# Performance work log

Hardware: AMD Instinct MI355X
Metric: run time of the kernel (lower is better)

## Reference

```python
import jax, jax.numpy as jnp
import numpy as np

EPS = 1e-5

def layer_norm(h, g, b):
    m = h.mean(-1, keepdims=True)
    v = ((h - m) ** 2).mean(-1, keepdims=True)
    return (h - m) * jax.lax.rsqrt(v + EPS) * g + b

def setup_inputs() -> dict:
    key = jax.random.key(0)
    ks = jax.random.split(key, 16)
    B, D, C, H, EH, L = 64, 20000, 16, 64, 128, 32
    s = lambda k, fan_in, shape: jax.random.normal(k, shape, jnp.float32) / np.sqrt(fan_in)
    return {
        "x": jax.random.normal(ks[0], (B, D), jnp.float32),
        "mask": jax.random.randint(ks[1], (B, D), 0, 2, jnp.int32),
        "feature_embedding": jax.random.normal(ks[2], (D, C), jnp.float32),
        # h_layer: Linear(1+C -> H), LN, ReLU, Linear(H -> C), LN, ReLU
        "W1": s(ks[3], 1 + C, (1 + C, H)), "b1": jnp.zeros((H,), jnp.float32),
        "g1": jnp.ones((H,), jnp.float32), "be1": jnp.zeros((H,), jnp.float32),
        "W2": s(ks[4], H, (H, C)), "b2": jnp.zeros((C,), jnp.float32),
        "g2": jnp.ones((C,), jnp.float32), "be2": jnp.zeros((C,), jnp.float32),
        # encoder_mlp (FCLayers, 2 layers, LayerNorm + ReLU each): C -> EH -> 2L
        "We1": s(ks[5], C, (C, EH)), "bb1": jnp.zeros((EH,), jnp.float32),
        "gg1": jnp.ones((EH,), jnp.float32), "bbe1": jnp.zeros((EH,), jnp.float32),
        "We2": s(ks[6], EH, (EH, 2 * L)), "bb2": jnp.zeros((2 * L,), jnp.float32),
        "gg2": jnp.ones((2 * L,), jnp.float32), "bbe2": jnp.zeros((2 * L,), jnp.float32),
    }

def reference(x, mask, feature_embedding, W1, b1, g1, be1, W2, b2, g2, be2,
              We1, bb1, gg1, bbe1, We2, bb2, gg2, bbe2):
    B, D = x.shape
    C = feature_embedding.shape[1]
    # per-feature point-net: h_layer runs row-wise, so we compute it densely
    # for all (b, d) and zero out unobserved entries before pooling —
    # identical math to the per-sample masked gather in the original.
    h_in = jnp.concatenate(
        [x[..., None], jnp.broadcast_to(feature_embedding, (B, D, C))], axis=-1
    )  # [B, D, 1+C]
    h = jax.nn.relu(layer_norm(h_in @ W1 + b1, g1, be1))   # [B, D, H]
    h = jax.nn.relu(layer_norm(h @ W2 + b2, g2, be2))      # [B, D, C]
    m = mask.astype(h.dtype)
    summed = jnp.einsum('bdc,bd->bc', h, m)                # masked sum pool
    num_obs = jnp.maximum(m.sum(axis=1, keepdims=True), 1.0)
    c = summed / num_obs                                   # pool_mode='mean'
    # encoder_mlp
    e = jax.nn.relu(layer_norm(c @ We1 + bb1, gg1, bbe1))
    e = jax.nn.relu(layer_norm(e @ We2 + bb2, gg2, bbe2))  # [B, 2*latent]
    mu, logvar = jnp.split(e, 2, axis=-1)
    return mu, logvar
```

## Files before the change

kernel.cpp:

```cpp
#include <hip/hip_runtime.h>
#include <hip/hip_bf16.h>

#define EPSF 1e-5f

namespace {
constexpr int B = 64, D = 20000, C = 16, H = 64, EH = 128, L = 32;
constexpr int CHUNK = 256;
constexpr int NCHUNK = (D + CHUNK - 1) / CHUNK;
constexpr int GX = 12;
}

typedef __attribute__((ext_vector_type(8))) short bf16x8;
typedef __attribute__((ext_vector_type(4))) float f32x4;

static __device__ __forceinline__ unsigned short f2bf(float f) {
    __hip_bfloat16 h = __float2bfloat16(f);
    return __builtin_bit_cast(unsigned short, h);
}
static __device__ __forceinline__ unsigned int packbf(float lo, float hi) {
    return ((unsigned int)f2bf(hi) << 16) | (unsigned int)f2bf(lo);
}

__global__ __launch_bounds__(256) void k_count_prep(
    const int* __restrict__ mask, const float* __restrict__ fe,
    const float* __restrict__ W1, const float* __restrict__ b1,
    const float* __restrict__ W2,
    int* __restrict__ chunkpop, unsigned short* __restrict__ febf,
    unsigned short* __restrict__ W1T, unsigned short* __restrict__ W2T)
{
    const int j = blockIdx.x, b = blockIdx.y;
    const int t = threadIdx.x;
    if (j < NCHUNK) {
        const int d = j * CHUNK + t;
        const int mv = (d < D) ? mask[(size_t)b * D + d] : 0;
        const unsigned long long bal = __ballot(mv != 0);
        __shared__ int ws[4];
        const int lane = t & 63, wid = t >> 6;
        if (lane == 0) ws[wid] = __popcll(bal);
        __syncthreads();
        if (t == 0) chunkpop[b * NCHUNK + j] = ws[0] + ws[1] + ws[2] + ws[3];
    } else {
        const int gtid = b * 256 + t;
        for (int u = gtid; u < (D * C) / 8; u += B * 256) {
            const float4 f0 = *(const float4*)(fe + (size_t)u * 8);
            const float4 f1 = *(const float4*)(fe + (size_t)u * 8 + 4);
            uint4 pk;
            pk.x = packbf(f0.x, f0.y); pk.y = packbf(f0.z, f0.w);
            pk.z = packbf(f1.x, f1.y); pk.w = packbf(f1.z, f1.w);
            *(uint4*)(febf + (size_t)u * 8) = pk;
        }
        if (b == 0) {
            for (int e = t; e < H * 32; e += 256) {
                const int h = e >> 5, kk = e & 31;
                float v = 0.f;
                if (kk < 16)       v = W1[(kk + 1) * H + h];
                else if (kk == 16) v = W1[h];
                else if (kk == 17) v = b1[h];
                W1T[e] = f2bf(v);
            }
        } else if (b == 1) {
            for (int e = t; e < C * H; e += 256) {
                const int c = e >> 6, hh = e & 63;
                W2T[e] = f2bf(W2[hh * C + c]);
            }
        }
    }
}

__global__ __launch_bounds__(256) void k_scatter(
    const int* __restrict__ mask, const int* __restrict__ chunkpop,
    unsigned short* __restrict__ cd, int* __restrict__ cnt)
{
    const int b = blockIdx.y, j = blockIdx.x;
    const int t = threadIdx.x;
    const int lane = t & 63, wid = t >> 6;

    int val = (t < NCHUNK) ? chunkpop[b * NCHUNK + t] : 0;
    int pre = (t < j) ? val : 0;
    #pragma unroll
    for (int off = 32; off > 0; off >>= 1) {
        val += __shfl_xor(val, off);
        pre += __shfl_xor(pre, off);
    }
    __shared__ int redv[4], redp[4], wc[4];
    if (lane == 0) { redv[wid] = val; redp[wid] = pre; }
    __syncthreads();
    const int total = redv[0] + redv[1] + redv[2] + redv[3];
    const int off0  = redp[0] + redp[1] + redp[2] + redp[3];
    if (j == 0 && t == 0) cnt[b] = total;

    const int d = j * CHUNK + t;
    const int mv = (d < D) ? mask[(size_t)b * D + d] : 0;
    const unsigned long long bal = __ballot(mv != 0);
    if (lane == 0) wc[wid] = __popcll(bal);
    __syncthreads();
    int woff = 0;
    for (int w2 = 0; w2 < wid; ++w2) woff += wc[w2];
    const int prel = __popcll(bal & ((1ull << lane) - 1ull));
    if (mv)
        cd[(size_t)b * D + off0 + woff + prel] = (unsigned short)d;
}

__global__ __launch_bounds__(256) void k_rows(
    const float* __restrict__ x, const unsigned short* __restrict__ cd,
    const int* __restrict__ cnt, const unsigned short* __restrict__ febf,
    const unsigned short* __restrict__ W1T, const unsigned short* __restrict__ W2T,
    const float* __restrict__ g1, const float* __restrict__ be1,
    const float* __restrict__ g2, const float* __restrict__ be2,
    const float* __restrict__ b2,
    float* __restrict__ part)
{
    const int b  = blockIdx.y;
    const int bx = blockIdx.x;
    const int n  = cnt[b];
    const int tid = threadIdx.x;
    const int w = tid >> 6, lane = tid & 63;
    const int g = lane >> 4, q = lane & 15;
    const size_t bD = (size_t)b * D;

    bf16x8 w1f[4];
    #pragma unroll
    for (int m = 0; m < 4; ++m)
        w1f[m] = *(const bf16x8*)(W1T + (16 * m + q) * 32 + 8 * g);
    bf16x8 w2f[2];
    #pragma unroll
    for (int ks = 0; ks < 2; ++ks)
        w2f[ks] = *(const bf16x8*)(W2T + q * 64 + 32 * ks + 8 * g);

    float4 g1v[4], be1v[4];
    #pragma unroll
    for (int m = 0; m < 4; ++m) {
        g1v[m]  = *(const float4*)(g1  + 16 * m + 4 * g);
        be1v[m] = *(const float4*)(be1 + 16 * m + 4 * g);
    }
    const float4 g2v  = *(const float4*)(g2  + 4 * g);
    const float4 be2v = *(const float4*)(be2 + 4 * g);
    const float4 b2v  = *(const float4*)(b2  + 4 * g);

    __shared__ __align__(16) unsigned short Rs[4][8][16][8];
    __shared__ float wsum[4][16];

    f32x4 acc = {0.f, 0.f, 0.f, 0.f};

    const int nch = (n + CHUNK - 1) / CHUNK;
    for (int j = bx; j < nch; j += GX) {
        const int cbase = j * CHUNK + w * 64;

        bf16x8 hb[4];
        #pragma unroll
        for (int it = 0; it < 4; ++it) {
            const int gb = cbase + it * 16;
            bf16x8 hv;
            #pragma unroll
            for (int e = 0; e < 8; ++e) hv[e] = 0;
            if (gb < n) {
                const int idx = gb + q;
                const bool v = idx < n;
                if (g < 2) {
                    int d = 0;
                    if (v) d = cd[bD + idx];
                    hv = *(const bf16x8*)(febf + (size_t)d * 16 + 8 * g);
                } else if (g == 2) {
                    float xv = 0.f;
                    if (v) { const int d = cd[bD + idx]; xv = x[bD + d]; }
                    hv[0] = (short)f2bf(xv);
                    hv[1] = (short)0x3F80;
                }
            }
            hb[it] = hv;
        }

        #pragma unroll
        for (int it = 0; it < 4; ++it) {
            const int gb = cbase + it * 16;
            if (gb >= n) continue;
            const f32x4 z = {0.f, 0.f, 0.f, 0.f};
            f32x4 t1a[4];
            #pragma unroll
            for (int m = 0; m < 4; ++m)
                t1a[m] = __builtin_amdgcn_mfma_f32_16x16x32_bf16(w1f[m], hb[it], z, 0, 0, 0);

            float s0 = 0.f, s1 = 0.f, q0 = 0.f, q1 = 0.f;
            #pragma unroll
            for (int m = 0; m < 4; ++m) {
                s0 += t1a[m][0] + t1a[m][1];
                s1 += t1a[m][2] + t1a[m][3];
                q0 = fmaf(t1a[m][0], t1a[m][0], fmaf(t1a[m][1], t1a[m][1], q0));
                q1 = fmaf(t1a[m][2], t1a[m][2], fmaf(t1a[m][3], t1a[m][3], q1));
            }
            float s = s0 + s1, sq = q0 + q1;
            s  += __shfl_xor(s, 16);  sq += __shfl_xor(sq, 16);
            s  += __shfl_xor(s, 32);  sq += __shfl_xor(sq, 32);
            const float mean1 = s * (1.f / H);
            const float var1  = fmaxf(sq * (1.f / H) - mean1 * mean1, 0.f);
            const float rstd1 = rsqrtf(var1 + EPSF);

            #pragma unroll
            for (int m = 0; m < 4; ++m) {
                const float v0 = fmaxf(fmaf((t1a[m][0] - mean1) * rstd1, g1v[m].x, be1v[m].x), 0.f);
                const float v1 = fmaxf(fmaf((t1a[m][1] - mean1) * rstd1, g1v[m].y, be1v[m].y), 0.f);
                const float v2 = fmaxf(fmaf((t1a[m][2] - mean1) * rstd1, g1v[m].z, be1v[m].z), 0.f);
                const float v3 = fmaxf(fmaf((t1a[m][3] - mean1) * rstd1, g1v[m].w, be1v[m].w), 0.f);
                uint2 pk = make_uint2(packbf(v0, v1), packbf(v2, v3));
                *(uint2*)&Rs[w][2 * m + (g >> 1)][q][4 * (g & 1)] = pk;
            }

            const bf16x8 rb0 = *(const bf16x8*)&Rs[w][g][q][0];
            const bf16x8 rb1 = *(const bf16x8*)&Rs[w][4 + g][q][0];
            f32x4 a2 = __builtin_amdgcn_mfma_f32_16x16x32_bf16(w2f[0], rb0, z, 0, 0, 0);
            a2 = __builtin_amdgcn_mfma_f32_16x16x32_bf16(w2f[1], rb1, a2, 0, 0, 0);
            a2[0] += b2v.x; a2[1] += b2v.y; a2[2] += b2v.z; a2[3] += b2v.w;

            float s2 = (a2[0] + a2[1]) + (a2[2] + a2[3]);
            float q2 = fmaf(a2[0], a2[0], fmaf(a2[1], a2[1],
                       fmaf(a2[2], a2[2], a2[3] * a2[3])));
            s2 += __shfl_xor(s2, 16);  q2 += __shfl_xor(q2, 16);
            s2 += __shfl_xor(s2, 32);  q2 += __shfl_xor(q2, 32);
            const float mean2 = s2 * (1.f / C);
            const float var2  = fmaxf(q2 * (1.f / C) - mean2 * mean2, 0.f);
            const float rstd2 = rsqrtf(var2 + EPSF);
            const float vm = (gb + q < n) ? 1.f : 0.f;
            acc[0] += fmaxf(fmaf((a2[0] - mean2) * rstd2, g2v.x, be2v.x), 0.f) * vm;
            acc[1] += fmaxf(fmaf((a2[1] - mean2) * rstd2, g2v.y, be2v.y), 0.f) * vm;
            acc[2] += fmaxf(fmaf((a2[2] - mean2) * rstd2, g2v.z, be2v.z), 0.f) * vm;
            acc[3] += fmaxf(fmaf((a2[3] - mean2) * rstd2, g2v.w, be2v.w), 0.f) * vm;
        }
    }

    #pragma unroll
    for (int off = 1; off < 16; off <<= 1) {
        #pragma unroll
        for (int r = 0; r < 4; ++r) acc[r] += __shfl_xor(acc[r], off);
    }
    if (q == 0)
        *(float4*)&wsum[w][4 * g] = make_float4(acc[0], acc[1], acc[2], acc[3]);
    __syncthreads();
    if (tid < C)
        part[((size_t)b * GX + bx) * C + tid] =
            wsum[0][tid] + wsum[1][tid] + wsum[2][tid] + wsum[3][tid];
}

__global__ __launch_bounds__(EH) void k_enc(
    const float* __restrict__ part, const int* __restrict__ cnt,
    const float* __restrict__ We1, const float* __restrict__ bb1,
    const float* __restrict__ gg1, const float* __restrict__ bbe1,
    const float* __restrict__ We2, const float* __restrict__ bb2,
    const float* __restrict__ gg2, const float* __restrict__ bbe2,
    float* __restrict__ out)
{
    const int b = blockIdx.x;
    const int t = threadIdx.x;
    __shared__ float cc[C];
    __shared__ float stats[2];
    __shared__ float buf[EH];
    __shared__ float buf2[2 * L];

    const int n = cnt[b];
    if (t < C) {
        float s = 0.f;
        #pragma unroll
        for (int j = 0; j < GX; ++j)
            s += part[((size_t)b * GX + j) * C + t];
        cc[t] = s;
    }
    __syncthreads();
    const float inv = 1.f / fmaxf((float)n, 1.f);

    float v1 = bb1[t];
    #pragma unroll
    for (int c = 0; c < C; ++c)
        v1 = fmaf(cc[c] * inv, We1[c * EH + t], v1);
    buf[t] = v1;
    __syncthreads();
    if (t == 0) {
        float s = 0.f, ss = 0.f;
        for (int j2 = 0; j2 < EH; ++j2) { s += buf[j2]; ss = fmaf(buf[j2], buf[j2], ss); }
        float mn = s * (1.f / EH);
        float vr = fmaxf(ss * (1.f / EH) - mn * mn, 0.f);
        stats[0] = mn; stats[1] = rsqrtf(vr + EPSF);
    }
    __syncthreads();
    float e1 = fmaxf(fmaf((v1 - stats[0]) * stats[1], gg1[t], bbe1[t]), 0.f);
    __syncthreads();
    buf[t] = e1;
    __syncthreads();

    float v2 = 0.f;
    if (t < 2 * L) {
        v2 = bb2[t];
        #pragma unroll
        for (int h = 0; h < EH; ++h)
            v2 = fmaf(buf[h], We2[h * (2 * L) + t], v2);
        buf2[t] = v2;
    }
    __syncthreads();
    if (t == 0) {
        float s = 0.f, ss = 0.f;
        for (int j2 = 0; j2 < 2 * L; ++j2) { s += buf2[j2]; ss = fmaf(buf2[j2], buf2[j2], ss); }
        float mn = s * (1.f / (2 * L));
        float vr = fmaxf(ss * (1.f / (2 * L)) - mn * mn, 0.f);
        stats[0] = mn; stats[1] = rsqrtf(vr + EPSF);
    }
    __syncthreads();
    if (t < 2 * L) {
        float e2 = fmaxf(fmaf((v2 - stats[0]) * stats[1], gg2[t], bbe2[t]), 0.f);
        if (t < L) out[(size_t)b * L + t]                       = e2;
        else       out[(size_t)B * L + (size_t)b * L + (t - L)] = e2;
    }
}

extern "C" void kernel_launch(void* const* d_in, const int* in_sizes, int n_in,
                              void* d_out, int out_size, void* d_ws, size_t ws_size,
                              hipStream_t stream) {
    const float* x    = (const float*)d_in[0];
    const int*   mask = (const int*)d_in[1];
    const float* fe   = (const float*)d_in[2];
    const float* W1   = (const float*)d_in[3];
    const float* b1   = (const float*)d_in[4];
    const float* g1   = (const float*)d_in[5];
    const float* be1  = (const float*)d_in[6];
    const float* W2   = (const float*)d_in[7];
    const float* b2   = (const float*)d_in[8];
    const float* g2   = (const float*)d_in[9];
    const float* be2  = (const float*)d_in[10];
    const float* We1  = (const float*)d_in[11];
    const float* bb1  = (const float*)d_in[12];
    const float* gg1  = (const float*)d_in[13];
    const float* bbe1 = (const float*)d_in[14];
    const float* We2  = (const float*)d_in[15];
    const float* bb2  = (const float*)d_in[16];
    const float* gg2  = (const float*)d_in[17];
    const float* bbe2 = (const float*)d_in[18];
    float* out = (float*)d_out;

    char* wp = (char*)d_ws;
    float* part     = (float*)wp;               wp += (size_t)B * GX * C * 4;
    int*   cnt      = (int*)wp;                 wp += (size_t)B * 4;
    int*   chunkpop = (int*)wp;                 wp += (size_t)B * NCHUNK * 4;
    unsigned short* W1T  = (unsigned short*)wp; wp += (size_t)H * 32 * 2;
    unsigned short* W2T  = (unsigned short*)wp; wp += (size_t)C * H * 2;
    unsigned short* febf = (unsigned short*)wp; wp += (size_t)D * C * 2;
    unsigned short* cd   = (unsigned short*)wp;

    hipLaunchKernelGGL(k_count_prep, dim3(NCHUNK + 1, B), dim3(256), 0, stream,
                       mask, fe, W1, b1, W2, chunkpop, febf, W1T, W2T);
    hipLaunchKernelGGL(k_scatter, dim3(NCHUNK, B), dim3(256), 0, stream,
                       mask, chunkpop, cd, cnt);
    hipLaunchKernelGGL(k_rows, dim3(GX, B), dim3(256), 0, stream,
                       x, cd, cnt, febf, W1T, W2T, g1, be1, g2, be2, b2, part);
    hipLaunchKernelGGL(k_enc, dim3(B), dim3(EH), 0, stream,
                       part, cnt, We1, bb1, gg1, bbe1, We2, bb2, gg2, bbe2, out);
}
```

Measured before the change: 51.01 us.

## Fuse mask count and scatter into single-pass per-row compaction kernel

Replaces the two-kernel count-then-scatter compaction with one kernel where each 1024-thread block serially scans one batch row of the mask, computing running offsets and writing compacted indices. This removes one launch and the chunkpop round trip. The trade-off is that only 64 blocks do the serial 20-iteration scan. It also raises the k_rows grid width from 12 to 26, adds a launch-bounds occupancy hint, and gives each unrolled iteration its own LDS staging slice to remove reuse hazards between iterations.

```diff
diff --git a/kernel.cpp b/kernel.cpp
--- a/kernel.cpp
+++ b/kernel.cpp
@@ -6,8 +6,8 @@
 namespace {
 constexpr int B = 64, D = 20000, C = 16, H = 64, EH = 128, L = 32;
 constexpr int CHUNK = 256;
-constexpr int NCHUNK = (D + CHUNK - 1) / CHUNK;
-constexpr int GX = 12;
+constexpr int GX = 26;
+constexpr int PB = 16;
 }
 
 typedef __attribute__((ext_vector_type(8))) short bf16x8;
@@ -21,27 +21,51 @@
     return ((unsigned int)f2bf(hi) << 16) | (unsigned int)f2bf(lo);
 }
 
-__global__ __launch_bounds__(256) void k_count_prep(
+__global__ __launch_bounds__(1024) void k_prep(
     const int* __restrict__ mask, const float* __restrict__ fe,
     const float* __restrict__ W1, const float* __restrict__ b1,
     const float* __restrict__ W2,
-    int* __restrict__ chunkpop, unsigned short* __restrict__ febf,
+    unsigned short* __restrict__ cd, int* __restrict__ cnt,
+    unsigned short* __restrict__ febf,
     unsigned short* __restrict__ W1T, unsigned short* __restrict__ W2T)
 {
-    const int j = blockIdx.x, b = blockIdx.y;
     const int t = threadIdx.x;
-    if (j < NCHUNK) {
-        const int d = j * CHUNK + t;
-        const int mv = (d < D) ? mask[(size_t)b * D + d] : 0;
-        const unsigned long long bal = __ballot(mv != 0);
-        __shared__ int ws[4];
+    if (blockIdx.x < B) {
+        const int b = blockIdx.x;
         const int lane = t & 63, wid = t >> 6;
-        if (lane == 0) ws[wid] = __popcll(bal);
-        __syncthreads();
-        if (t == 0) chunkpop[b * NCHUNK + j] = ws[0] + ws[1] + ws[2] + ws[3];
+        __shared__ int wc[16];
+        const size_t bD = (size_t)b * D;
+        constexpr int NIT = (D + 1023) / 1024;
+        int mv = (t < D) ? mask[bD + t] : 0;
+        int base = 0;
+        for (int it = 0; it < NIT; ++it) {
+            int mv_next = 0;
+            const int dn = (it + 1) * 1024 + t;
+            if (it + 1 < NIT && dn < D) mv_next = mask[bD + dn];
+            const unsigned long long bal = __ballot(mv != 0);
+            if (lane == 0) wc[wid] = __popcll(bal);
+            __syncthreads();
+            int woff = 0, tot = 0;
+            #pragma unroll
+            for (int k2 = 0; k2 < 16; ++k2) {
+                const int c0 = wc[k2];
+                tot += c0;
+                if (k2 < wid) woff += c0;
+            }
+            if (mv) {
+                const int d = it * 1024 + t;
+                const int pre = __popcll(bal & ((1ull << lane) - 1ull));
+                cd[bD + base + woff + pre] = (unsigned short)d;
+            }
+            base += tot;
+            __syncthreads();
+            mv = mv_next;
+        }
+        if (t == 0) cnt[b] = base;
     } else {
-        const int gtid = b * 256 + t;
-        for (int u = gtid; u < (D * C) / 8; u += B * 256) {
+        const int pb = blockIdx.x - B;
+        const int gtid = pb * 1024 + t;
+        for (int u = gtid; u < (D * C) / 8; u += PB * 1024) {
             const float4 f0 = *(const float4*)(fe + (size_t)u * 8);
             const float4 f1 = *(const float4*)(fe + (size_t)u * 8 + 4);
             uint4 pk;
@@ -49,8 +73,8 @@
             pk.z = packbf(f1.x, f1.y); pk.w = packbf(f1.z, f1.w);
             *(uint4*)(febf + (size_t)u * 8) = pk;
         }
-        if (b == 0) {
-            for (int e = t; e < H * 32; e += 256) {
+        if (pb == 0) {
+            for (int e = t; e < H * 32; e += 1024) {
                 const int h = e >> 5, kk = e & 31;
                 float v = 0.f;
                 if (kk < 16)       v = W1[(kk + 1) * H + h];
@@ -58,50 +82,16 @@
                 else if (kk == 17) v = b1[h];
                 W1T[e] = f2bf(v);
             }
-        } else if (b == 1) {
-            for (int e = t; e < C * H; e += 256) {
-                const int c = e >> 6, hh = e & 63;
-                W2T[e] = f2bf(W2[hh * C + c]);
-            }
-        }
-    }
-}
-
-__global__ __launch_bounds__(256) void k_scatter(
-    const int* __restrict__ mask, const int* __restrict__ chunkpop,
-    unsigned short* __restrict__ cd, int* __restrict__ cnt)
-{
-    const int b = blockIdx.y, j = blockIdx.x;
-    const int t = threadIdx.x;
-    const int lane = t & 63, wid = t >> 6;
-
-    int val = (t < NCHUNK) ? chunkpop[b * NCHUNK + t] : 0;
-    int pre = (t < j) ? val : 0;
-    #pragma unroll
-    for (int off = 32; off > 0; off >>= 1) {
-        val += __shfl_xor(val, off);
-        pre += __shfl_xor(pre, off);
-    }
-    __shared__ int redv[4], redp[4], wc[4];
-    if (lane == 0) { redv[wid] = val; redp[wid] = pre; }
-    __syncthreads();
-    const int total = redv[0] + redv[1] + redv[2] + redv[3];
-    const int off0  = redp[0] + redp[1] + redp[2] + redp[3];
-    if (j == 0 && t == 0) cnt[b] = total;
-
-    const int d = j * CHUNK + t;
-    const int mv = (d < D) ? mask[(size_t)b * D + d] : 0;
-    const unsigned long long bal = __ballot(mv != 0);
-    if (lane == 0) wc[wid] = __popcll(bal);
-    __syncthreads();
-    int woff = 0;
-    for (int w2 = 0; w2 < wid; ++w2) woff += wc[w2];
-    const int prel = __popcll(bal & ((1ull << lane) - 1ull));
-    if (mv)
-        cd[(size_t)b * D + off0 + woff + prel] = (unsigned short)d;
-}
-
-__global__ __launch_bounds__(256) void k_rows(
+        } else if (pb == 1) {
+            for (int e = t; e < C * H; e += 1024) {
+                const int c0 = e >> 6, hh = e & 63;
+                W2T[e] = f2bf(W2[hh * C + c0]);
+            }
+        }
+    }
+}
+
+__global__ __launch_bounds__(256, 4) void k_rows(
     const float* __restrict__ x, const unsigned short* __restrict__ cd,
     const int* __restrict__ cnt, const unsigned short* __restrict__ febf,
     const unsigned short* __restrict__ W1T, const unsigned short* __restrict__ W2T,
@@ -137,7 +127,7 @@
     const float4 be2v = *(const float4*)(be2 + 4 * g);
     const float4 b2v  = *(const float4*)(b2  + 4 * g);
 
-    __shared__ __align__(16) unsigned short Rs[4][8][16][8];
+    __shared__ __align__(16) unsigned short Rs[4][4][8][16][8];
     __shared__ float wsum[4][16];
 
     f32x4 acc = {0.f, 0.f, 0.f, 0.f};
@@ -202,11 +192,11 @@
                 const float v2 = fmaxf(fmaf((t1a[m][2] - mean1) * rstd1, g1v[m].z, be1v[m].z), 0.f);
                 const float v3 = fmaxf(fmaf((t1a[m][3] - mean1) * rstd1, g1v[m].w, be1v[m].w), 0.f);
                 uint2 pk = make_uint2(packbf(v0, v1), packbf(v2, v3));
-                *(uint2*)&Rs[w][2 * m + (g >> 1)][q][4 * (g & 1)] = pk;
-            }
-
-            const bf16x8 rb0 = *(const bf16x8*)&Rs[w][g][q][0];
-            const bf16x8 rb1 = *(const bf16x8*)&Rs[w][4 + g][q][0];
+                *(uint2*)&Rs[w][it][2 * m + (g >> 1)][q][4 * (g & 1)] = pk;
+            }
+
+            const bf16x8 rb0 = *(const bf16x8*)&Rs[w][it][g][q][0];
+            const bf16x8 rb1 = *(const bf16x8*)&Rs[w][it][4 + g][q][0];
             f32x4 a2 = __builtin_amdgcn_mfma_f32_16x16x32_bf16(w2f[0], rb0, z, 0, 0, 0);
             a2 = __builtin_amdgcn_mfma_f32_16x16x32_bf16(w2f[1], rb1, a2, 0, 0, 0);
             a2[0] += b2v.x; a2[1] += b2v.y; a2[2] += b2v.z; a2[3] += b2v.w;
@@ -336,16 +326,13 @@
     char* wp = (char*)d_ws;
     float* part     = (float*)wp;               wp += (size_t)B * GX * C * 4;
     int*   cnt      = (int*)wp;                 wp += (size_t)B * 4;
-    int*   chunkpop = (int*)wp;                 wp += (size_t)B * NCHUNK * 4;
     unsigned short* W1T  = (unsigned short*)wp; wp += (size_t)H * 32 * 2;
     unsigned short* W2T  = (unsigned short*)wp; wp += (size_t)C * H * 2;
     unsigned short* febf = (unsigned short*)wp; wp += (size_t)D * C * 2;
     unsigned short* cd   = (unsigned short*)wp;
 
-    hipLaunchKernelGGL(k_count_prep, dim3(NCHUNK + 1, B), dim3(256), 0, stream,
-                       mask, fe, W1, b1, W2, chunkpop, febf, W1T, W2T);
-    hipLaunchKernelGGL(k_scatter, dim3(NCHUNK, B), dim3(256), 0, stream,
-                       mask, chunkpop, cd, cnt);
+    hipLaunchKernelGGL(k_prep, dim3(B + PB), dim3(1024), 0, stream,
+                       mask, fe, W1, b1, W2, cd, cnt, febf, W1T, W2T);
     hipLaunchKernelGGL(k_rows, dim3(GX, B), dim3(256), 0, stream,
                        x, cd, cnt, febf, W1T, W2T, g1, be1, g2, be2, b2, part);
     hipLaunchKernelGGL(k_enc, dim3(B), dim3(EH), 0, stream,
```

After: 54.73 us. +7.3%, slower.
